# Optimization experiments

Hardware: AMD Instinct MI355X
Metric: run time of the kernel (lower is better)

## Reference

```python
import jax, jax.numpy as jnp
import numpy as np

K = 5  # number of nearest triangles (init kwarg k)
EPS = 1e-6


def setup_inputs() -> dict:
    key = jax.random.key(0)
    k1, k2, k3, k4 = jax.random.split(key, 4)
    V, F, S = 4000, 6000, 10
    sampled_vertices = jax.random.normal(k1, (V, 3), dtype=jnp.float32)
    simplified_faces = jax.random.randint(k2, (F, 3), 0, V, dtype=jnp.int64)
    u = jax.random.uniform(k3, (F, S, 1), dtype=jnp.float32)
    v = jax.random.uniform(k4, (F, S, 1), dtype=jnp.float32)
    return {"sampled_vertices": sampled_vertices, "simplified_faces": simplified_faces,
            "u": u, "v": v}


def reference(sampled_vertices, simplified_faces, u, v):
    verts = sampled_vertices          # [V,3]
    faces = simplified_faces          # [F,3]

    # --- sample_points_from_triangles (reflect (u,v) into the triangle) ---
    cond = (u + v) > 1.0
    uu = jnp.where(cond, 1.0 - u, u)  # [F,S,1]
    vv = jnp.where(cond, 1.0 - v, v)
    v0 = verts[faces[:, 0]]           # [F,3]
    v1 = verts[faces[:, 1]]
    v2 = verts[faces[:, 2]]
    points = (v0[:, None] * (1.0 - uu - vv) + v1[:, None] * uu + v2[:, None] * vv)
    P = points.reshape(-1, 3)         # [N,3], N = F*S

    # --- find_nearest_triangles: cdist + topk (smallest) ---
    centroids = verts[faces].mean(axis=1)                 # [F,3]
    # squared euclidean distance; same ordering as torch.cdist for topk
    d2 = (jnp.sum(P * P, -1)[:, None]
          + jnp.sum(centroids * centroids, -1)[None, :]
          - 2.0 * P @ centroids.T)                        # [N,F]
    _, idx = jax.lax.top_k(-d2, K)                        # [N,K]

    # --- vectorized barycentric containment test over all (point, tri) pairs ---
    tri = faces[idx]                  # [N,K,3]
    tv = verts[tri]                   # [N,K,3,3]
    a, b, c = tv[:, :, 0], tv[:, :, 1], tv[:, :, 2]       # [N,K,3]
    n = jnp.cross(b - a, c - a)                           # [N,K,3]
    area = 0.5 * jnp.linalg.norm(n, axis=-1)              # [N,K]
    p = P[:, None, :]                                     # [N,1,3]
    uc = jnp.sum(jnp.cross(c - b, p - b) * n, axis=-1)
    vc = jnp.sum(jnp.cross(a - c, p - c) * n, axis=-1)
    wc = jnp.sum(jnp.cross(b - a, p - a) * n, axis=-1)
    inside = (jnp.abs(area) > EPS) & (uc >= 0) & (vc >= 0) & (wc >= 0)
    return jnp.sum(jnp.where(inside, area, 0.0))
```

## Files before the change

kernel.cpp:

```cpp
#include <hip/hip_runtime.h>
#include <float.h>

#define KNN   5
#define FEPS  1e-6f
#define NSAMP 10
#define NWAVE 8
#define PPB   64

static __device__ __forceinline__ unsigned umn(unsigned a, unsigned b){ return __builtin_elementwise_min(a, b); }
static __device__ __forceinline__ unsigned umx(unsigned a, unsigned b){ return __builtin_elementwise_max(a, b); }
static __device__ __forceinline__ unsigned med3u(unsigned a, unsigned b, unsigned c){
    unsigned r; asm("v_med3_u32 %0, %1, %2, %3" : "=v"(r) : "v"(a), "v"(b), "v"(c)); return r;
}

__global__ __launch_bounds__(256) void centroid_kernel(
    const float* __restrict__ verts, const int* __restrict__ faces,
    float4* __restrict__ cent, int F, int Fpad)
{
    int i = blockIdx.x * blockDim.x + threadIdx.x;
    if (i < F) {
        int i0 = faces[3*i], i1 = faces[3*i+1], i2 = faces[3*i+2];
        float cx = (verts[3*i0+0] + verts[3*i1+0] + verts[3*i2+0]) * (1.0f/3.0f);
        float cy = (verts[3*i0+1] + verts[3*i1+1] + verts[3*i2+1]) * (1.0f/3.0f);
        float cz = (verts[3*i0+2] + verts[3*i1+2] + verts[3*i2+2]) * (1.0f/3.0f);
        float h  = fmaf(cx, cx, fmaf(cy, cy, cz*cz));
        cent[i] = make_float4(cx, cy, cz, h);
    } else if (i < Fpad) {
        cent[i] = make_float4(0.0f, 0.0f, 0.0f, 3.0e38f);
    }
}

__global__ __launch_bounds__(512, 8) void scan_kernel(
    const float* __restrict__ verts, const int* __restrict__ faces,
    const float* __restrict__ uarr, const float* __restrict__ varr,
    const float4* __restrict__ cent,
    float* __restrict__ out, int CH, int N)
{
    __shared__ unsigned cand[KNN][NWAVE][64];
    __shared__ float wsum[NWAVE];

    const int  lane  = threadIdx.x & 63;
    const int  w     = threadIdx.x >> 6;
    const int  p     = blockIdx.x * PPB + lane;
    const bool valid = p < N;
    const int  pc    = valid ? p : N - 1;

    float uu = uarr[pc], vv = varr[pc];
    if (uu + vv > 1.0f) { uu = 1.0f - uu; vv = 1.0f - vv; }
    float w0 = 1.0f - uu - vv;
    int  f  = pc / NSAMP;
    int  i0 = faces[3*f], i1 = faces[3*f+1], i2 = faces[3*f+2];
    float px = verts[3*i0+0]*w0 + verts[3*i1+0]*uu + verts[3*i2+0]*vv;
    float py = verts[3*i0+1]*w0 + verts[3*i1+1]*uu + verts[3*i2+1]*vv;
    float pz = verts[3*i0+2]*w0 + verts[3*i1+2]*uu + verts[3*i2+2]*vv;
    float qx = -2.0f*px, qy = -2.0f*py, qz = -2.0f*pz;
    float pp = fmaf(px, px, fmaf(py, py, pz*pz));

    const int c0 = __builtin_amdgcn_readfirstlane(CH * w);
    const float4* __restrict__ cw = cent + c0;

    unsigned maskv;
    asm("v_mov_b32 %0, 0xFFFFE000" : "=v"(maskv));

    unsigned k0=0xFFFFFFFFu,k1=0xFFFFFFFFu,k2=0xFFFFFFFFu,k3=0xFFFFFFFFu,k4=0xFFFFFFFFu;

    #pragma unroll 4
    for (int t = 0; t < CH; t += 2) {
        float4 ca = cw[t];
        float4 cb = cw[t+1];
        float ha = ca.w + pp;
        float hb = cb.w + pp;
        float sa = fmaf(qx, ca.x, fmaf(qy, ca.y, fmaf(qz, ca.z, ha)));
        float sb = fmaf(qx, cb.x, fmaf(qy, cb.y, fmaf(qz, cb.z, hb)));
        unsigned ua, ub;
        asm("v_bfi_b32 %0, %1, %2, %3" : "=v"(ua)
            : "v"(maskv), "v"(__float_as_uint(sa)), "s"(c0 + t));
        asm("v_bfi_b32 %0, %1, %2, %3" : "=v"(ub)
            : "v"(maskv), "v"(__float_as_uint(sb)), "s"(c0 + t + 1));
        unsigned wm = umn(ua, ub);
        unsigned lm = umx(ua, ub);
        {
            unsigned n4 = med3u(k3, k4, wm);
            unsigned n3 = med3u(k2, k3, wm);
            unsigned n2 = med3u(k1, k2, wm);
            unsigned n1 = med3u(k0, k1, wm);
            k0 = umn(k0, wm); k1 = n1; k2 = n2; k3 = n3; k4 = n4;
        }
        if (__any(lm < k4)) {
            unsigned n4 = med3u(k3, k4, lm);
            unsigned n3 = med3u(k2, k3, lm);
            unsigned n2 = med3u(k1, k2, lm);
            unsigned n1 = med3u(k0, k1, lm);
            k0 = umn(k0, lm); k1 = n1; k2 = n2; k3 = n3; k4 = n4;
        }
    }

    cand[0][w][lane] = k0;
    cand[1][w][lane] = k1;
    cand[2][w][lane] = k2;
    cand[3][w][lane] = k3;
    cand[4][w][lane] = k4;
    __syncthreads();

    float psum = 0.0f;
    if (valid && w < KNN) {
        unsigned m0=0xFFFFFFFFu,m1=0xFFFFFFFFu,m2=0xFFFFFFFFu,m3=0xFFFFFFFFu,m4=0xFFFFFFFFu;
        for (int cw2 = 0; cw2 < NWAVE; ++cw2) {
            #pragma unroll
            for (int k = 0; k < KNN; ++k) {
                unsigned u = cand[k][cw2][lane];
                unsigned n4 = med3u(m3, m4, u);
                unsigned n3 = med3u(m2, m3, u);
                unsigned n2 = med3u(m1, m2, u);
                unsigned n1 = med3u(m0, m1, u);
                m0 = umn(m0, u); m1 = n1; m2 = n2; m3 = n3; m4 = n4;
            }
        }
        unsigned mw = (w == 0) ? m0 : (w == 1) ? m1 : (w == 2) ? m2 : (w == 3) ? m3 : m4;
        int fj = (int)(mw & 0x1FFFu);

        int a0 = faces[3*fj], a1 = faces[3*fj+1], a2 = faces[3*fj+2];
        float ax = verts[3*a0+0], ay = verts[3*a0+1], az = verts[3*a0+2];
        float bx = verts[3*a1+0], by = verts[3*a1+1], bz = verts[3*a1+2];
        float cx = verts[3*a2+0], cy = verts[3*a2+1], cz = verts[3*a2+2];

        float e1x = bx-ax, e1y = by-ay, e1z = bz-az;
        float e2x = cx-ax, e2y = cy-ay, e2z = cz-az;
        float nx = e1y*e2z - e1z*e2y;
        float ny = e1z*e2x - e1x*e2z;
        float nz = e1x*e2y - e1y*e2x;
        float area = 0.5f * sqrtf(nx*nx + ny*ny + nz*nz);

        float cbx = cx-bx, cby = cy-by, cbz = cz-bz;
        float pbx = px-bx, pby = py-by, pbz = pz-bz;
        float uc = (cby*pbz - cbz*pby)*nx + (cbz*pbx - cbx*pbz)*ny + (cbx*pby - cby*pbx)*nz;

        float acx = ax-cx, acy = ay-cy, acz = az-cz;
        float pcx = px-cx, pcy = py-cy, pcz = pz-cz;
        float vc = (acy*pcz - acz*pcy)*nx + (acz*pcx - acx*pcz)*ny + (acx*pcy - acy*pcx)*nz;

        float pax = px-ax, pay = py-ay, paz = pz-az;
        float wc = (e1y*paz - e1z*pay)*nx + (e1z*pax - e1x*paz)*ny + (e1x*pay - e1y*pax)*nz;

        if (fabsf(area) > FEPS && uc >= 0.0f && vc >= 0.0f && wc >= 0.0f)
            psum = area;
    }

    #pragma unroll
    for (int off = 32; off > 0; off >>= 1)
        psum += __shfl_down(psum, off, 64);
    if (lane == 0) wsum[w] = psum;
    __syncthreads();
    if (threadIdx.x == 0) {
        float t = 0.0f;
        #pragma unroll
        for (int i = 0; i < NWAVE; ++i) t += wsum[i];
        atomicAdd(out, t);
    }
}

extern "C" void kernel_launch(void* const* d_in, const int* in_sizes, int n_in,
                              void* d_out, int out_size, void* d_ws, size_t ws_size,
                              hipStream_t stream) {
    const float* verts = (const float*)d_in[0];
    const int*   faces = (const int*)d_in[1];
    const float* u     = (const float*)d_in[2];
    const float* v     = (const float*)d_in[3];
    float*       out   = (float*)d_out;
    float4*      cent  = (float4*)d_ws;

    int F = in_sizes[1] / 3;
    int N = in_sizes[2];
    int Fpad = ((F + NWAVE*8 - 1) / (NWAVE*8)) * (NWAVE*8);
    int CH   = Fpad / NWAVE;

    hipMemsetAsync(d_out, 0, sizeof(float), stream);
    centroid_kernel<<<(Fpad + 255) / 256, 256, 0, stream>>>(verts, faces, cent, F, Fpad);
    int blocks = (N + PPB - 1) / PPB;
    scan_kernel<<<blocks, 512, 0, stream>>>(verts, faces, u, v, cent, out, CH, N);
}
```

Baseline: 104.1 us.

## Store centroids as SoA and compute distance pairs with packed FP32 math

Centroids are now stored in four separate arrays (x, y, z, squared norm) instead of float4. The scan loop loads pairs of each component as 64-bit scalar values and computes two distances at once using v_pk_add_f32 and v_pk_fma_f32. This halves the number of distance ALU instructions in the hot loop. The risks are the fixed CSTRIDE of 6144, which limits Fpad, and the assumption that the compiler keeps the 64-bit loads uniform in SGPRs as the inline asm requires.

```diff
diff --git a/kernel.cpp b/kernel.cpp
--- a/kernel.cpp
+++ b/kernel.cpp
@@ -7,6 +7,14 @@
 #define NWAVE 8
 #define PPB   64
 
+#define CSTRIDE 6144
+#define OFF_X   0
+#define OFF_Y   (CSTRIDE*4)
+#define OFF_Z   (CSTRIDE*8)
+#define OFF_W   (CSTRIDE*12)
+
+typedef __attribute__((ext_vector_type(2))) float f32x2;
+
 static __device__ __forceinline__ unsigned umn(unsigned a, unsigned b){ return __builtin_elementwise_min(a, b); }
 static __device__ __forceinline__ unsigned umx(unsigned a, unsigned b){ return __builtin_elementwise_max(a, b); }
 static __device__ __forceinline__ unsigned med3u(unsigned a, unsigned b, unsigned c){
@@ -15,7 +23,8 @@
 
 __global__ __launch_bounds__(256) void centroid_kernel(
     const float* __restrict__ verts, const int* __restrict__ faces,
-    float4* __restrict__ cent, int F, int Fpad)
+    float* __restrict__ X, float* __restrict__ Y, float* __restrict__ Z,
+    float* __restrict__ W, int F, int Fpad)
 {
     int i = blockIdx.x * blockDim.x + threadIdx.x;
     if (i < F) {
@@ -24,16 +33,17 @@
         float cy = (verts[3*i0+1] + verts[3*i1+1] + verts[3*i2+1]) * (1.0f/3.0f);
         float cz = (verts[3*i0+2] + verts[3*i1+2] + verts[3*i2+2]) * (1.0f/3.0f);
         float h  = fmaf(cx, cx, fmaf(cy, cy, cz*cz));
-        cent[i] = make_float4(cx, cy, cz, h);
+        X[i] = cx; Y[i] = cy; Z[i] = cz; W[i] = h;
     } else if (i < Fpad) {
-        cent[i] = make_float4(0.0f, 0.0f, 0.0f, 3.0e38f);
+        X[i] = 0.0f; Y[i] = 0.0f; Z[i] = 0.0f; W[i] = 3.0e38f;
     }
 }
 
 __global__ __launch_bounds__(512, 8) void scan_kernel(
     const float* __restrict__ verts, const int* __restrict__ faces,
     const float* __restrict__ uarr, const float* __restrict__ varr,
-    const float4* __restrict__ cent,
+    const float* __restrict__ X, const float* __restrict__ Y,
+    const float* __restrict__ Z, const float* __restrict__ W,
     float* __restrict__ out, int CH, int N)
 {
     __shared__ unsigned cand[KNN][NWAVE][64];
@@ -56,8 +66,13 @@
     float qx = -2.0f*px, qy = -2.0f*py, qz = -2.0f*pz;
     float pp = fmaf(px, px, fmaf(py, py, pz*pz));
 
+    f32x2 qx2 = {qx, qx}, qy2 = {qy, qy}, qz2 = {qz, qz}, pp2 = {pp, pp};
+
     const int c0 = __builtin_amdgcn_readfirstlane(CH * w);
-    const float4* __restrict__ cw = cent + c0;
+    const float* __restrict__ Xw = X + c0;
+    const float* __restrict__ Yw = Y + c0;
+    const float* __restrict__ Zw = Z + c0;
+    const float* __restrict__ Ww = W + c0;
 
     unsigned maskv;
     asm("v_mov_b32 %0, 0xFFFFE000" : "=v"(maskv));
@@ -66,17 +81,20 @@
 
     #pragma unroll 4
     for (int t = 0; t < CH; t += 2) {
-        float4 ca = cw[t];
-        float4 cb = cw[t+1];
-        float ha = ca.w + pp;
-        float hb = cb.w + pp;
-        float sa = fmaf(qx, ca.x, fmaf(qy, ca.y, fmaf(qz, ca.z, ha)));
-        float sb = fmaf(qx, cb.x, fmaf(qy, cb.y, fmaf(qz, cb.z, hb)));
+        unsigned long long X2 = *(const unsigned long long*)(Xw + t);
+        unsigned long long Y2 = *(const unsigned long long*)(Yw + t);
+        unsigned long long Z2 = *(const unsigned long long*)(Zw + t);
+        unsigned long long W2 = *(const unsigned long long*)(Ww + t);
+        f32x2 acc;
+        asm("v_pk_add_f32 %0, %1, %2"     : "=v"(acc) : "s"(W2), "v"(pp2));
+        asm("v_pk_fma_f32 %0, %1, %2, %3" : "=v"(acc) : "v"(qz2), "s"(Z2), "v"(acc));
+        asm("v_pk_fma_f32 %0, %1, %2, %3" : "=v"(acc) : "v"(qy2), "s"(Y2), "v"(acc));
+        asm("v_pk_fma_f32 %0, %1, %2, %3" : "=v"(acc) : "v"(qx2), "s"(X2), "v"(acc));
         unsigned ua, ub;
         asm("v_bfi_b32 %0, %1, %2, %3" : "=v"(ua)
-            : "v"(maskv), "v"(__float_as_uint(sa)), "s"(c0 + t));
+            : "v"(maskv), "v"(__float_as_uint(acc[0])), "s"(c0 + t));
         asm("v_bfi_b32 %0, %1, %2, %3" : "=v"(ub)
-            : "v"(maskv), "v"(__float_as_uint(sb)), "s"(c0 + t + 1));
+            : "v"(maskv), "v"(__float_as_uint(acc[1])), "s"(c0 + t + 1));
         unsigned wm = umn(ua, ub);
         unsigned lm = umx(ua, ub);
         {
@@ -167,7 +185,12 @@
     const float* u     = (const float*)d_in[2];
     const float* v     = (const float*)d_in[3];
     float*       out   = (float*)d_out;
-    float4*      cent  = (float4*)d_ws;
+    char*        ws    = (char*)d_ws;
+
+    float* X = (float*)(ws + OFF_X);
+    float* Y = (float*)(ws + OFF_Y);
+    float* Z = (float*)(ws + OFF_Z);
+    float* W = (float*)(ws + OFF_W);
 
     int F = in_sizes[1] / 3;
     int N = in_sizes[2];
@@ -175,7 +198,7 @@
     int CH   = Fpad / NWAVE;
 
     hipMemsetAsync(d_out, 0, sizeof(float), stream);
-    centroid_kernel<<<(Fpad + 255) / 256, 256, 0, stream>>>(verts, faces, cent, F, Fpad);
+    centroid_kernel<<<(Fpad + 255) / 256, 256, 0, stream>>>(verts, faces, X, Y, Z, W, F, Fpad);
     int blocks = (N + PPB - 1) / PPB;
-    scan_kernel<<<blocks, 512, 0, stream>>>(verts, faces, u, v, cent, out, CH, N);
-}
+    scan_kernel<<<blocks, 512, 0, stream>>>(verts, faces, u, v, X, Y, Z, W, out, CH, N);
+}
```

New measurement: 123.1 us. 1.18x slower.
